# Optimization experiments

Hardware: AMD Instinct MI355X
Metric: run time of the kernel (lower is better)

## Reference

```python
import jax, jax.numpy as jnp
import numpy as np


def setup_inputs() -> dict:
    key = jax.random.key(0)
    k1, k2 = jax.random.split(key)
    B, Lq, Lk, D = 4, 4096, 4096, 512
    query = jax.random.normal(k1, (B, Lq, D), dtype=jnp.float32)
    value = jax.random.normal(k2, (B, Lk, D), dtype=jnp.float32)
    return {"query": query, "value": value}


def reference(query, value):
    # score: [B, Lq, Lk] = query @ value^T (unscaled, unmasked)
    score = jnp.einsum('bqd,bkd->bqk', query, value)
    attn = jax.nn.softmax(score, axis=-1)
    # context: [B, Lq, D]
    context = jnp.einsum('bqk,bkd->bqd', attn, value)
    return (context, attn)
```

## Files before the change

### kernel.cpp

```cpp
#include <hip/hip_runtime.h>
#include <cstddef>
#include <cstdint>

typedef unsigned short u16;

constexpr int BATCH = 4;
constexpr int Lq = 4096;
constexpr int Lk = 4096;
constexpr int D  = 512;

constexpr int BM = 128, BN = 128, BK = 32;
constexpr int LDA = 40;

using bf16x8 = __attribute__((ext_vector_type(8))) short;
using f32x4  = __attribute__((ext_vector_type(4))) float;

__device__ inline u16 f32_to_bf16_rne(float x) {
    uint32_t u = __builtin_bit_cast(uint32_t, x);
    u += 0x7fff + ((u >> 16) & 1);
    return (u16)(u >> 16);
}
__device__ inline float bf16_bits_to_f32(u16 h) {
    uint32_t u = ((uint32_t)h) << 16;
    return __builtin_bit_cast(float, u);
}
__device__ inline void split2(float x, float y, uint32_t& hi, uint32_t& lo) {
    u16 hx = f32_to_bf16_rne(x);
    u16 hy = f32_to_bf16_rne(y);
    u16 lx = f32_to_bf16_rne(x - bf16_bits_to_f32(hx));
    u16 ly = f32_to_bf16_rne(y - bf16_bits_to_f32(hy));
    hi = (uint32_t)hx | ((uint32_t)hy << 16);
    lo = (uint32_t)lx | ((uint32_t)ly << 16);
}
__device__ inline uint32_t pack2_bf16(float x, float y) {
    return (uint32_t)f32_to_bf16_rne(x) | ((uint32_t)f32_to_bf16_rne(y) << 16);
}
__device__ inline void gld16(const u16* g, u16* l) {
    __builtin_amdgcn_global_load_lds(
        (const __attribute__((address_space(1))) void*)g,
        (__attribute__((address_space(3))) void*)l, 16, 0, 0);
}
__device__ inline f32x4 mfma16(bf16x8 a, bf16x8 b, f32x4 c) {
    return __builtin_amdgcn_mfma_f32_16x16x32_bf16(a, b, c, 0, 0, 0);
}

__global__ __launch_bounds__(256)
void split_bf16(const float* __restrict__ src, u16* __restrict__ hi,
                u16* __restrict__ lo, int n4)
{
    const int i = blockIdx.x * 256 + threadIdx.x;
    if (i >= n4) return;
    const float4 v = ((const float4*)src)[i];
    uint2 h, l;
    split2(v.x, v.y, h.x, l.x);
    split2(v.z, v.w, h.y, l.y);
    ((uint2*)hi)[i] = h;
    ((uint2*)lo)[i] = l;
}

__global__ __launch_bounds__(256)
void transpose_v_bf16(const float* __restrict__ V, u16* __restrict__ VT)
{
    __shared__ float tile[32][33];
    const int b = blockIdx.z;
    const float* in = V + (size_t)b * Lk * D;
    u16* out = VT + (size_t)b * D * Lk;
    const int lk0 = blockIdx.x * 32;
    const int d0  = blockIdx.y * 32;
    const int c  = threadIdx.x & 31;
    const int r0 = threadIdx.x >> 5;
    #pragma unroll
    for (int i = 0; i < 4; ++i) {
        const int r = r0 + 8 * i;
        tile[r][c] = in[(size_t)(lk0 + r) * D + d0 + c];
    }
    __syncthreads();
    #pragma unroll
    for (int i = 0; i < 4; ++i) {
        const int r = r0 + 8 * i;
        out[(size_t)(d0 + r) * Lk + lk0 + c] = f32_to_bf16_rne(tile[c][r]);
    }
}

__global__ __launch_bounds__(512, 2)
void gemm1_8p(const u16* __restrict__ Qhi, const u16* __restrict__ Qlo,
              const u16* __restrict__ Vhi, const u16* __restrict__ Vlo,
              float* __restrict__ Sg)
{
    constexpr int K  = D;
    constexpr int NT = K / 32;
    __shared__ u16 lds[2 * 4 * 8192];

    const int b = blockIdx.z;
    const u16* Ah = Qhi + (size_t)b * Lq * K;
    const u16* Al = Qlo + (size_t)b * Lq * K;
    const u16* Bh = Vhi + (size_t)b * Lk * K;
    const u16* Bl = Vlo + (size_t)b * Lk * K;
    float* C = Sg + (size_t)b * Lq * Lk;

    const int m0 = blockIdx.y * 256;
    const int n0 = blockIdx.x * 256;
    const int t = threadIdx.x, lane = t & 63, w = t >> 6;
    const int wm = (w >> 2) * 128, wn = (w & 3) * 64;
    const int fr = lane & 15, fq = lane >> 4;

    const int cg   = (lane & 3) ^ ((lane >> 3) & 3);
    const int rsub = lane >> 2;
    const int offA0 = (m0 + w * 32 + rsub) * K + cg * 8;
    const int offA1 = offA0 + 16 * K;
    const int offB0 = (n0 + w * 32 + rsub) * K + cg * 8;
    const int offB1 = offB0 + 16 * K;
    const int ch = w * 1024;

    const int swzc = fq ^ ((fr >> 1) & 3);
    const int aRd = (wm + fr) * 64 + swzc * 16;
    const int bRd = (wn + fr) * 64 + swzc * 16;

    f32x4 acc[8][4] = {};
    bf16x8 aH[4], aL[4], bH[4], bL[4];

    {
        u16* a = &lds[ch];
        gld16(Ah + offA0, a);
        gld16(Ah + offA1, a + 512);
        gld16(Al + offA0, a + 8192);
        gld16(Al + offA1, a + 8192 + 512);
        u16* v = &lds[16384 + ch];
        gld16(Bh + offB0, v);
        gld16(Bh + offB1, v + 512);
        gld16(Bl + offB0, v + 8192);
        gld16(Bl + offB1, v + 8192 + 512);
    }
    asm volatile("s_waitcnt vmcnt(0)" ::: "memory");
    __builtin_amdgcn_s_barrier();
    __builtin_amdgcn_sched_barrier(0);

    for (int kt = 0; kt < NT; ++kt) {
        const int cur = kt & 1;
        const char* ls = (const char*)lds + cur * 65536;
        const int kn = (kt + 1) * 32;
        const int nb = (cur ^ 1) * 32768;

        #pragma unroll
        for (int m = 0; m < 4; ++m) {
            aH[m] = *(const bf16x8*)(ls + aRd + m * 1024);
            aL[m] = *(const bf16x8*)(ls + 16384 + aRd + m * 1024);
        }
        #pragma unroll
        for (int n = 0; n < 2; ++n) {
            bH[n] = *(const bf16x8*)(ls + 32768 + bRd + n * 1024);
            bL[n] = *(const bf16x8*)(ls + 49152 + bRd + n * 1024);
        }
        if (kt < NT - 1) {
            u16* a = &lds[nb + ch];
            gld16(Ah + offA0 + kn, a);
            gld16(Ah + offA1 + kn, a + 512);
            gld16(Al + offA0 + kn, a + 8192);
            gld16(Al + offA1 + kn, a + 8192 + 512);
        }
        __builtin_amdgcn_s_barrier();
        asm volatile("s_waitcnt lgkmcnt(0)" ::: "memory");
        __builtin_amdgcn_sched_barrier(0);
        __builtin_amdgcn_s_setprio(1);
        #pragma unroll
        for (int m = 0; m < 4; ++m)
            #pragma unroll
            for (int n = 0; n < 2; ++n) {
                acc[m][n] = mfma16(aH[m], bH[n], acc[m][n]);
                acc[m][n] = mfma16(aH[m], bL[n], acc[m][n]);
                acc[m][n] = mfma16(aL[m], bH[n], acc[m][n]);
            }
        __builtin_amdgcn_s_setprio(0);
        __builtin_amdgcn_s_barrier();
        __builtin_amdgcn_sched_barrier(0);

        #pragma unroll
        for (int n = 2; n < 4; ++n) {
            bH[n] = *(const bf16x8*)(ls + 32768 + bRd + n * 1024);
            bL[n] = *(const bf16x8*)(ls + 49152 + bRd + n * 1024);
        }
        if (kt < NT - 1) {
            u16* v = &lds[nb + 16384 + ch];
            gld16(Bh + offB0 + kn, v);
            gld16(Bh + offB1 + kn, v + 512);
            gld16(Bl + offB0 + kn, v + 8192);
            gld16(Bl + offB1 + kn, v + 8192 + 512);
        }
        __builtin_amdgcn_s_barrier();
        asm volatile("s_waitcnt lgkmcnt(0)" ::: "memory");
        __builtin_amdgcn_sched_barrier(0);
        __builtin_amdgcn_s_setprio(1);
        #pragma unroll
        for (int m = 0; m < 4; ++m)
            #pragma unroll
            for (int n = 2; n < 4; ++n) {
                acc[m][n] = mfma16(aH[m], bH[n], acc[m][n]);
                acc[m][n] = mfma16(aH[m], bL[n], acc[m][n]);
                acc[m][n] = mfma16(aL[m], bH[n], acc[m][n]);
            }
        __builtin_amdgcn_s_setprio(0);
        __builtin_amdgcn_s_barrier();
        __builtin_amdgcn_sched_barrier(0);

        #pragma unroll
        for (int m = 0; m < 4; ++m) {
            aH[m] = *(const bf16x8*)(ls + 4096 + aRd + m * 1024);
            aL[m] = *(const bf16x8*)(ls + 16384 + 4096 + aRd + m * 1024);
        }
        __builtin_amdgcn_s_barrier();
        asm volatile("s_waitcnt lgkmcnt(0)" ::: "memory");
        __builtin_amdgcn_sched_barrier(0);
        __builtin_amdgcn_s_setprio(1);
        #pragma unroll
        for (int m = 0; m < 4; ++m)
            #pragma unroll
            for (int n = 0; n < 2; ++n) {
                acc[4 + m][n] = mfma16(aH[m], bH[n], acc[4 + m][n]);
                acc[4 + m][n] = mfma16(aH[m], bL[n], acc[4 + m][n]);
                acc[4 + m][n] = mfma16(aL[m], bH[n], acc[4 + m][n]);
            }
        __builtin_amdgcn_s_setprio(0);
        __builtin_amdgcn_s_barrier();
        __builtin_amdgcn_sched_barrier(0);

        __builtin_amdgcn_s_setprio(1);
        #pragma unroll
        for (int m = 0; m < 4; ++m)
            #pragma unroll
            for (int n = 2; n < 4; ++n) {
                acc[4 + m][n] = mfma16(aH[m], bH[n], acc[4 + m][n]);
                acc[4 + m][n] = mfma16(aH[m], bL[n], acc[4 + m][n]);
                acc[4 + m][n] = mfma16(aL[m], bH[n], acc[4 + m][n]);
            }
        __builtin_amdgcn_s_setprio(0);
        asm volatile("s_waitcnt vmcnt(0)" ::: "memory");
        __builtin_amdgcn_s_barrier();
        __builtin_amdgcn_sched_barrier(0);
    }

    const int rowb = m0 + wm + fq * 4;
    const int colb = n0 + wn + fr;
    #pragma unroll
    for (int mi = 0; mi < 8; ++mi)
        #pragma unroll
        for (int ni = 0; ni < 4; ++ni)
            #pragma unroll
            for (int r = 0; r < 4; ++r)
                C[(size_t)(rowb + mi * 16 + r) * Lk + colb + ni * 16] = acc[mi][ni][r];
}

__global__ __launch_bounds__(256)
void softmax_inplace(float* __restrict__ S, u16* __restrict__ Pb)
{
    const size_t row = blockIdx.x;
    float* p = S + row * (size_t)Lk;
    const int t = threadIdx.x;

    float4 v[4];
    #pragma unroll
    for (int i = 0; i < 4; ++i) v[i] = ((const float4*)p)[t + i * 256];

    float m = -3.0e38f;
    #pragma unroll
    for (int i = 0; i < 4; ++i)
        m = fmaxf(m, fmaxf(fmaxf(v[i].x, v[i].y), fmaxf(v[i].z, v[i].w)));
    #pragma unroll
    for (int off = 32; off > 0; off >>= 1) m = fmaxf(m, __shfl_xor(m, off));
    __shared__ float redm[4];
    if ((t & 63) == 0) redm[t >> 6] = m;
    __syncthreads();
    m = fmaxf(fmaxf(redm[0], redm[1]), fmaxf(redm[2], redm[3]));

    float s = 0.f;
    #pragma unroll
    for (int i = 0; i < 4; ++i) {
        v[i].x = __expf(v[i].x - m); s += v[i].x;
        v[i].y = __expf(v[i].y - m); s += v[i].y;
        v[i].z = __expf(v[i].z - m); s += v[i].z;
        v[i].w = __expf(v[i].w - m); s += v[i].w;
    }
    #pragma unroll
    for (int off = 32; off > 0; off >>= 1) s += __shfl_xor(s, off);
    __shared__ float reds[4];
    if ((t & 63) == 0) reds[t >> 6] = s;
    __syncthreads();
    s = (reds[0] + reds[1]) + (reds[2] + reds[3]);

    const float inv = 1.0f / s;
    u16* prow = Pb ? Pb + row * (size_t)Lk : nullptr;
    #pragma unroll
    for (int i = 0; i < 4; ++i) {
        v[i].x *= inv; v[i].y *= inv; v[i].z *= inv; v[i].w *= inv;
        ((float4*)p)[t + i * 256] = v[i];
        if (prow) {
            ushort4 h = make_ushort4(f32_to_bf16_rne(v[i].x), f32_to_bf16_rne(v[i].y),
                                     f32_to_bf16_rne(v[i].z), f32_to_bf16_rne(v[i].w));
            ((ushort4*)prow)[t + i * 256] = h;
        }
    }
}

__global__ __launch_bounds__(256, 3)
void gemm2_mfma(const u16* __restrict__ Pg, const u16* __restrict__ VTg,
                float* __restrict__ Cg)
{
    constexpr int K = Lk;
    constexpr int N = D;
    __shared__ u16 sA[BM * BK];
    __shared__ u16 sB[BN * BK];

    const int b = blockIdx.z;
    const u16* A  = Pg  + (size_t)b * Lq * Lk;
    const u16* Bp = VTg + (size_t)b * (size_t)D * Lk;
    float* C = Cg + (size_t)b * Lq * D;

    const int m0 = blockIdx.y * BM;
    const int n0 = blockIdx.x * BN;
    const int t = threadIdx.x, lane = t & 63, wave = t >> 6;
    const int wm = (wave >> 1) * 64, wn = (wave & 1) * 64;
    const int fr = lane & 15, fq = lane >> 4;

    const int r0  = wave * 16 + (lane >> 2);
    const int r1  = r0 + 64;
    const int kc8 = (lane & 3) * 8;
    const int oA0 = (m0 + r0) * K + kc8;
    const int oA1 = (m0 + r1) * K + kc8;
    const int oB0 = (n0 + r0) * K + kc8;
    const int oB1 = (n0 + r1) * K + kc8;
    const int w0 = wave * 512, w1 = (wave + 4) * 512;

    f32x4 acc[4][4] = {};

    for (int k0 = 0; k0 < K; k0 += BK) {
        if (k0) __syncthreads();
        gld16(A  + oA0 + k0, &sA[w0]);
        gld16(A  + oA1 + k0, &sA[w1]);
        gld16(Bp + oB0 + k0, &sB[w0]);
        gld16(Bp + oB1 + k0, &sB[w1]);
        __syncthreads();

        bf16x8 af[4], bf[4];
        #pragma unroll
        for (int x = 0; x < 4; ++x) {
            af[x] = *(const bf16x8*)&sA[(wm + x * 16 + fr) * BK + fq * 8];
            bf[x] = *(const bf16x8*)&sB[(wn + x * 16 + fr) * BK + fq * 8];
        }
        #pragma unroll
        for (int mi = 0; mi < 4; ++mi)
            #pragma unroll
            for (int ni = 0; ni < 4; ++ni)
                acc[mi][ni] = __builtin_amdgcn_mfma_f32_16x16x32_bf16(af[mi], bf[ni], acc[mi][ni], 0, 0, 0);
    }

    #pragma unroll
    for (int mi = 0; mi < 4; ++mi)
        #pragma unroll
        for (int ni = 0; ni < 4; ++ni)
            #pragma unroll
            for (int r = 0; r < 4; ++r) {
                const int row = m0 + wm + mi * 16 + fq * 4 + r;
                const int col = n0 + wn + ni * 16 + fr;
                C[(size_t)row * N + col] = acc[mi][ni][r];
            }
}

__global__ __launch_bounds__(256, 2)
void gemm1_r2(const float* __restrict__ Qg, const float* __restrict__ Vg,
              float* __restrict__ Sg)
{
    constexpr int K = D;
    __shared__ alignas(16) u16 sAhi[BM * LDA];
    __shared__ alignas(16) u16 sAlo[BM * LDA];
    __shared__ alignas(16) u16 sBhi[BN * LDA];
    __shared__ alignas(16) u16 sBlo[BN * LDA];

    const int b = blockIdx.z;
    const float* A  = Qg + (size_t)b * Lq * D;
    const float* Bp = Vg + (size_t)b * Lk * D;
    float* C = Sg + (size_t)b * Lq * Lk;

    const int m0 = blockIdx.y * BM;
    const int n0 = blockIdx.x * BN;
    const int t = threadIdx.x, lane = t & 63, wave = t >> 6;
    const int wm = (wave >> 1) * 64, wn = (wave & 1) * 64;
    const int fr = lane & 15, fq = lane >> 4;
    const int sm = t >> 3, sc = t & 7;

    f32x4 acc[4][4] = {};

    for (int k0 = 0; k0 < K; k0 += BK) {
        if (k0) __syncthreads();
        #pragma unroll
        for (int i = 0; i < 4; ++i) {
            const int m = sm + 32 * i;
            const float4 va = *(const float4*)(A  + (size_t)(m0 + m) * K + k0 + sc * 4);
            const float4 vb = *(const float4*)(Bp + (size_t)(n0 + m) * K + k0 + sc * 4);
            uint2 h, l;
            split2(va.x, va.y, h.x, l.x);
            split2(va.z, va.w, h.y, l.y);
            *(uint2*)&sAhi[m * LDA + sc * 4] = h;
            *(uint2*)&sAlo[m * LDA + sc * 4] = l;
            split2(vb.x, vb.y, h.x, l.x);
            split2(vb.z, vb.w, h.y, l.y);
            *(uint2*)&sBhi[m * LDA + sc * 4] = h;
            *(uint2*)&sBlo[m * LDA + sc * 4] = l;
        }
        __syncthreads();

        bf16x8 ah[4], al[4], bh[4], bl[4];
        #pragma unroll
        for (int x = 0; x < 4; ++x) {
            ah[x] = *(const bf16x8*)&sAhi[(wm + x * 16 + fr) * LDA + fq * 8];
            al[x] = *(const bf16x8*)&sAlo[(wm + x * 16 + fr) * LDA + fq * 8];
            bh[x] = *(const bf16x8*)&sBhi[(wn + x * 16 + fr) * LDA + fq * 8];
            bl[x] = *(const bf16x8*)&sBlo[(wn + x * 16 + fr) * LDA + fq * 8];
        }
        #pragma unroll
        for (int mi = 0; mi < 4; ++mi)
            #pragma unroll
            for (int ni = 0; ni < 4; ++ni) {
                acc[mi][ni] = __builtin_amdgcn_mfma_f32_16x16x32_bf16(ah[mi], bh[ni], acc[mi][ni], 0, 0, 0);
                acc[mi][ni] = __builtin_amdgcn_mfma_f32_16x16x32_bf16(ah[mi], bl[ni], acc[mi][ni], 0, 0, 0);
                acc[mi][ni] = __builtin_amdgcn_mfma_f32_16x16x32_bf16(al[mi], bh[ni], acc[mi][ni], 0, 0, 0);
            }
    }

    #pragma unroll
    for (int mi = 0; mi < 4; ++mi)
        #pragma unroll
        for (int ni = 0; ni < 4; ++ni)
            #pragma unroll
            for (int r = 0; r < 4; ++r) {
                const int row = m0 + wm + mi * 16 + fq * 4 + r;
                const int col = n0 + wn + ni * 16 + fr;
                C[(size_t)row * Lk + col] = acc[mi][ni][r];
            }
}

__global__ __launch_bounds__(256, 2)
void gemm2_r2(const float* __restrict__ Pg, const u16* __restrict__ VTg,
              float* __restrict__ Cg)
{
    constexpr int K = Lk;
    constexpr int N = D;
    __shared__ alignas(16) u16 sA[BM * LDA];
    __shared__ alignas(16) u16 sB[BN * LDA];

    const int b = blockIdx.z;
    const float* A  = Pg  + (size_t)b * Lq * Lk;
    const u16*   Bp = VTg + (size_t)b * (size_t)D * Lk;
    float* C = Cg + (size_t)b * Lq * D;

    const int m0 = blockIdx.y * BM;
    const int n0 = blockIdx.x * BN;
    const int t = threadIdx.x, lane = t & 63, wave = t >> 6;
    const int wm = (wave >> 1) * 64, wn = (wave & 1) * 64;
    const int fr = lane & 15, fq = lane >> 4;
    const int sm = t >> 3, sc = t & 7;
    const int bn = t >> 2, bc = t & 3;

    f32x4 acc[4][4] = {};

    for (int k0 = 0; k0 < K; k0 += BK) {
        if (k0) __syncthreads();
        #pragma unroll
        for (int i = 0; i < 4; ++i) {
            const int m = sm + 32 * i;
            const float4 va = *(const float4*)(A + (size_t)(m0 + m) * K + k0 + sc * 4);
            uint2 h;
            h.x = pack2_bf16(va.x, va.y);
            h.y = pack2_bf16(va.z, va.w);
            *(uint2*)&sA[m * LDA + sc * 4] = h;
        }
        #pragma unroll
        for (int i = 0; i < 2; ++i) {
            const int n = bn + 64 * i;
            const bf16x8 vb = *(const bf16x8*)(Bp + (size_t)(n0 + n) * K + k0 + bc * 8);
            *(bf16x8*)&sB[n * LDA + bc * 8] = vb;
        }
        __syncthreads();

        bf16x8 af[4], bf[4];
        #pragma unroll
        for (int x = 0; x < 4; ++x) {
            af[x] = *(const bf16x8*)&sA[(wm + x * 16 + fr) * LDA + fq * 8];
            bf[x] = *(const bf16x8*)&sB[(wn + x * 16 + fr) * LDA + fq * 8];
        }
        #pragma unroll
        for (int mi = 0; mi < 4; ++mi)
            #pragma unroll
            for (int ni = 0; ni < 4; ++ni)
                acc[mi][ni] = __builtin_amdgcn_mfma_f32_16x16x32_bf16(af[mi], bf[ni], acc[mi][ni], 0, 0, 0);
    }

    #pragma unroll
    for (int mi = 0; mi < 4; ++mi)
        #pragma unroll
        for (int ni = 0; ni < 4; ++ni)
            #pragma unroll
            for (int r = 0; r < 4; ++r) {
                const int row = m0 + wm + mi * 16 + fq * 4 + r;
                const int col = n0 + wn + ni * 16 + fr;
                C[(size_t)row * N + col] = acc[mi][ni][r];
            }
}

extern "C" void kernel_launch(void* const* d_in, const int* in_sizes, int n_in,
                              void* d_out, int out_size, void* d_ws, size_t ws_size,
                              hipStream_t stream)
{
    const float* Q = (const float*)d_in[0];
    const float* V = (const float*)d_in[1];
    float* ctx  = (float*)d_out;
    float* attn = (float*)d_out + (size_t)BATCH * Lq * D;

    constexpr size_t NQ = (size_t)BATCH * Lq * D;
    constexpr size_t NP = (size_t)BATCH * Lq * Lk;
    const size_t need = (5 * NQ + NP) * sizeof(u16);

    if (ws_size >= need) {
        u16* Qhi = (u16*)d_ws;
        u16* Qlo = Qhi + NQ;
        u16* Vhi = Qlo + NQ;
        u16* Vlo = Vhi + NQ;
        u16* VT  = Vlo + NQ;
        u16* Pb  = VT  + NQ;

        const int n4 = (int)(NQ / 4);
        split_bf16<<<dim3(n4 / 256), 256, 0, stream>>>(Q, Qhi, Qlo, n4);
        split_bf16<<<dim3(n4 / 256), 256, 0, stream>>>(V, Vhi, Vlo, n4);
        transpose_v_bf16<<<dim3(Lk / 32, D / 32, BATCH), 256, 0, stream>>>(V, VT);
        gemm1_8p<<<dim3(Lk / 256, Lq / 256, BATCH), 512, 0, stream>>>(Qhi, Qlo, Vhi, Vlo, attn);
        softmax_inplace<<<dim3(BATCH * Lq), 256, 0, stream>>>(attn, Pb);
        gemm2_mfma<<<dim3(D / BN, Lq / BM, BATCH), 256, 0, stream>>>(Pb, VT, ctx);
    } else {
        u16* VT = (u16*)d_ws;
        transpose_v_bf16<<<dim3(Lk / 32, D / 32, BATCH), 256, 0, stream>>>(V, VT);
        gemm1_r2<<<dim3(Lk / BN, Lq / BM, BATCH), 256, 0, stream>>>(Q, V, attn);
        softmax_inplace<<<dim3(BATCH * Lq), 256, 0, stream>>>(attn, nullptr);
        gemm2_r2<<<dim3(D / BN, Lq / BM, BATCH), 256, 0, stream>>>(attn, VT, ctx);
    }
}
```

Measured before the change: 740.6 us.

## Fuse Q/V split kernels, use wave-per-row softmax, widen gemm2 K tile with swizzle

Merges the two bf16 split launches into one kernel. Replaces the block-per-row softmax with one row per wavefront, dropping the shared-memory reductions and barriers at the cost of more registers per thread. Doubles the gemm2 K tile to 64 with an XOR-swizzled LDS layout, halving barrier count per K and reducing bank conflicts, while using more LDS per block.

```diff
diff --git a/kernel.cpp b/kernel.cpp
--- a/kernel.cpp
+++ b/kernel.cpp
@@ -45,11 +45,15 @@
 }
 
 __global__ __launch_bounds__(256)
-void split_bf16(const float* __restrict__ src, u16* __restrict__ hi,
-                u16* __restrict__ lo, int n4)
-{
-    const int i = blockIdx.x * 256 + threadIdx.x;
-    if (i >= n4) return;
+void split_qv_bf16(const float* __restrict__ Q, const float* __restrict__ V,
+                   u16* __restrict__ Qhi, u16* __restrict__ Qlo,
+                   u16* __restrict__ Vhi, u16* __restrict__ Vlo, int n4)
+{
+    int i = blockIdx.x * 256 + threadIdx.x;
+    const float* src;
+    u16 *hi, *lo;
+    if (i < n4) { src = Q; hi = Qhi; lo = Qlo; }
+    else        { src = V; hi = Vhi; lo = Vlo; i -= n4; }
     const float4 v = ((const float4*)src)[i];
     uint2 h, l;
     split2(v.x, v.y, h.x, l.x);
@@ -250,52 +254,44 @@
 }
 
 __global__ __launch_bounds__(256)
-void softmax_inplace(float* __restrict__ S, u16* __restrict__ Pb)
-{
-    const size_t row = blockIdx.x;
+void softmax_wave(float* __restrict__ S, u16* __restrict__ Pb)
+{
+    const size_t row = (size_t)blockIdx.x * 4 + (threadIdx.x >> 6);
+    const int l = threadIdx.x & 63;
     float* p = S + row * (size_t)Lk;
-    const int t = threadIdx.x;
-
-    float4 v[4];
-    #pragma unroll
-    for (int i = 0; i < 4; ++i) v[i] = ((const float4*)p)[t + i * 256];
+
+    float4 v[16];
+    #pragma unroll
+    for (int j = 0; j < 16; ++j) v[j] = ((const float4*)p)[l + j * 64];
 
     float m = -3.0e38f;
     #pragma unroll
-    for (int i = 0; i < 4; ++i)
-        m = fmaxf(m, fmaxf(fmaxf(v[i].x, v[i].y), fmaxf(v[i].z, v[i].w)));
+    for (int j = 0; j < 16; ++j)
+        m = fmaxf(m, fmaxf(fmaxf(v[j].x, v[j].y), fmaxf(v[j].z, v[j].w)));
     #pragma unroll
     for (int off = 32; off > 0; off >>= 1) m = fmaxf(m, __shfl_xor(m, off));
-    __shared__ float redm[4];
-    if ((t & 63) == 0) redm[t >> 6] = m;
-    __syncthreads();
-    m = fmaxf(fmaxf(redm[0], redm[1]), fmaxf(redm[2], redm[3]));
 
     float s = 0.f;
     #pragma unroll
-    for (int i = 0; i < 4; ++i) {
-        v[i].x = __expf(v[i].x - m); s += v[i].x;
-        v[i].y = __expf(v[i].y - m); s += v[i].y;
-        v[i].z = __expf(v[i].z - m); s += v[i].z;
-        v[i].w = __expf(v[i].w - m); s += v[i].w;
+    for (int j = 0; j < 16; ++j) {
+        v[j].x = __expf(v[j].x - m); s += v[j].x;
+        v[j].y = __expf(v[j].y - m); s += v[j].y;
+        v[j].z = __expf(v[j].z - m); s += v[j].z;
+        v[j].w = __expf(v[j].w - m); s += v[j].w;
     }
     #pragma unroll
     for (int off = 32; off > 0; off >>= 1) s += __shfl_xor(s, off);
-    __shared__ float reds[4];
-    if ((t & 63) == 0) reds[t >> 6] = s;
-    __syncthreads();
-    s = (reds[0] + reds[1]) + (reds[2] + reds[3]);
 
     const float inv = 1.0f / s;
     u16* prow = Pb ? Pb + row * (size_t)Lk : nullptr;
     #pragma unroll
-    for (int i = 0; i < 4; ++i) {
-        v[i].x *= inv; v[i].y *= inv; v[i].z *= inv; v[i].w *= inv;
-        ((float4*)p)[t + i * 256] = v[i];
+    for (int j = 0; j < 16; ++j) {
+        v[j].x *= inv; v[j].y *= inv; v[j].z *= inv; v[j].w *= inv;
+        ((float4*)p)[l + j * 64] = v[j];
         if (prow) {
-            ushort4 h = make_ushort4(f32_to_bf16_rne(v[i].x), f32_to_bf16_rne(v[i].y),
-                                     f32_to_bf16_rne(v[i].z), f32_to_bf16_rne(v[i].w));
-            ((ushort4*)prow)[t + i * 256] = h;
+            ushort4 h = make_ushort4(f32_to_bf16_rne(v[j].x), f32_to_bf16_rne(v[j].y),
+                                     f32_to_bf16_rne(v[j].z), f32_to_bf16_rne(v[j].w));
+            ((ushort4*)prow)[l + j * 64] = h;
         }
     }
 }
@@ -306,8 +302,8 @@
 {
     constexpr int K = Lk;
     constexpr int N = D;
-    __shared__ u16 sA[BM * BK];
-    __shared__ u16 sB[BN * BK];
+    __shared__ u16 sA[BM * 64];
+    __shared__ u16 sB[BN * 64];
 
     const int b = blockIdx.z;
     const u16* A  = Pg  + (size_t)b * Lq * Lk;
@@ -320,36 +316,38 @@
     const int wm = (wave >> 1) * 64, wn = (wave & 1) * 64;
     const int fr = lane & 15, fq = lane >> 4;
 
-    const int r0  = wave * 16 + (lane >> 2);
-    const int r1  = r0 + 64;
-    const int kc8 = (lane & 3) * 8;
-    const int oA0 = (m0 + r0) * K + kc8;
-    const int oA1 = (m0 + r1) * K + kc8;
-    const int oB0 = (n0 + r0) * K + kc8;
-    const int oB1 = (n0 + r1) * K + kc8;
-    const int w0 = wave * 512, w1 = (wave + 4) * 512;
+    const int lr  = lane >> 3;
+    const int gck = (lane & 7) ^ lr;
+    const int gA  = (m0 + wave * 32 + lr) * K + gck * 8;
+    const int gB  = (n0 + wave * 32 + lr) * K + gck * 8;
 
     f32x4 acc[4][4] = {};
 
-    for (int k0 = 0; k0 < K; k0 += BK) {
+    for (int k0 = 0; k0 < K; k0 += 64) {
         if (k0) __syncthreads();
-        gld16(A  + oA0 + k0, &sA[w0]);
-        gld16(A  + oA1 + k0, &sA[w1]);
-        gld16(Bp + oB0 + k0, &sB[w0]);
-        gld16(Bp + oB1 + k0, &sB[w1]);
+        #pragma unroll
+        for (int j = 0; j < 4; ++j) {
+            gld16(A  + gA + j * 8 * K + k0, &sA[(wave * 4 + j) * 512]);
+            gld16(Bp + gB + j * 8 * K + k0, &sB[(wave * 4 + j) * 512]);
+        }
         __syncthreads();
 
-        bf16x8 af[4], bf[4];
-        #pragma unroll
-        for (int x = 0; x < 4; ++x) {
-            af[x] = *(const bf16x8*)&sA[(wm + x * 16 + fr) * BK + fq * 8];
-            bf[x] = *(const bf16x8*)&sB[(wn + x * 16 + fr) * BK + fq * 8];
-        }
-        #pragma unroll
-        for (int mi = 0; mi < 4; ++mi)
-            #pragma unroll
-            for (int ni = 0; ni < 4; ++ni)
-                acc[mi][ni] = __builtin_amdgcn_mfma_f32_16x16x32_bf16(af[mi], bf[ni], acc[mi][ni], 0, 0, 0);
+        #pragma unroll
+        for (int ks = 0; ks < 2; ++ks) {
+            bf16x8 af[4], bf[4];
+            #pragma unroll
+            for (int x = 0; x < 4; ++x) {
+                const int ra = wm + x * 16 + fr;
+                const int rb = wn + x * 16 + fr;
+                af[x] = *(const bf16x8*)&sA[ra * 64 + ((ks * 4 + fq) ^ (ra & 7)) * 8];
+                bf[x] = *(const bf16x8*)&sB[rb * 64 + ((ks * 4 + fq) ^ (rb & 7)) * 8];
+            }
+            #pragma unroll
+            for (int mi = 0; mi < 4; ++mi)
+                #pragma unroll
+                for (int ni = 0; ni < 4; ++ni)
+                    acc[mi][ni] = mfma16(af[mi], bf[ni], acc[mi][ni]);
+        }
     }
 
     #pragma unroll
@@ -527,17 +525,16 @@
         u16* Pb  = VT  + NQ;
 
         const int n4 = (int)(NQ / 4);
-        split_bf16<<<dim3(n4 / 256), 256, 0, stream>>>(Q, Qhi, Qlo, n4);
-        split_bf16<<<dim3(n4 / 256), 256, 0, stream>>>(V, Vhi, Vlo, n4);
+        split_qv_bf16<<<dim3(2 * n4 / 256), 256, 0, stream>>>(Q, V, Qhi, Qlo, Vhi, Vlo, n4);
         transpose_v_bf16<<<dim3(Lk / 32, D / 32, BATCH), 256, 0, stream>>>(V, VT);
         gemm1_8p<<<dim3(Lk / 256, Lq / 256, BATCH), 512, 0, stream>>>(Qhi, Qlo, Vhi, Vlo, attn);
-        softmax_inplace<<<dim3(BATCH * Lq), 256, 0, stream>>>(attn, Pb);
+        softmax_wave<<<dim3(BATCH * Lq / 4), 256, 0, stream>>>(attn, Pb);
         gemm2_mfma<<<dim3(D / BN, Lq / BM, BATCH), 256, 0, stream>>>(Pb, VT, ctx);
     } else {
         u16* VT = (u16*)d_ws;
         transpose_v_bf16<<<dim3(Lk / 32, D / 32, BATCH), 256, 0, stream>>>(V, VT);
         gemm1_r2<<<dim3(Lk / BN, Lq / BM, BATCH), 256, 0, stream>>>(Q, V, attn);
-        softmax_inplace<<<dim3(BATCH * Lq), 256, 0, stream>>>(attn, nullptr);
+        softmax_wave<<<dim3(BATCH * Lq / 4), 256, 0, stream>>>(attn, nullptr);
         gemm2_r2<<<dim3(D / BN, Lq / BM, BATCH), 256, 0, stream>>>(attn, VT, ctx);
     }
 }
```

Result: no change. 727.0 us (-1.8%).
